# Kernel tuning notes

Measured on AMD Instinct MI355X. Metric: run time of the kernel, lower is better.

The kernel has to match this reference:

```python
import jax, jax.numpy as jnp
import numpy as np

N_NODES = 100000
N_EDGES = 800000
H_DIM = 128
E_DIM = 32
N_LAYER = 3


def setup_inputs() -> dict:
    key = jax.random.key(0)
    ks = jax.random.split(key, 5)
    x = jax.random.normal(ks[0], (N_NODES, H_DIM), dtype=jnp.float32)
    edge_index = jax.random.randint(ks[1], (2, N_EDGES), 0, N_NODES, dtype=jnp.int64)
    edge_attr = jax.random.normal(ks[2], (N_EDGES, E_DIM), dtype=jnp.float32)
    fan_in = 2 * H_DIM + E_DIM
    # torch Linear weight layout: [out_features, in_features]
    Wm = jax.random.normal(ks[3], (N_LAYER, H_DIM, fan_in), dtype=jnp.float32) / jnp.sqrt(fan_in)
    bm = jax.random.normal(ks[4], (N_LAYER, H_DIM), dtype=jnp.float32) * 0.01
    return {"x": x, "edge_index": edge_index, "edge_attr": edge_attr, "Wm": Wm, "bm": bm}


def reference(x, edge_index, edge_attr, Wm, bm):
    # PyG flow='source_to_target': row 0 = source (j), row 1 = target (i)
    src = edge_index[0]
    dst = edge_index[1]
    n_nodes = x.shape[0]
    n_layer = Wm.shape[0]
    for l in range(n_layer):  # small fixed layer count
        # message: m_ij = Linear(cat[x_j, x_i, edge_attr])
        m = jnp.concatenate([x[src], x[dst], edge_attr], axis=1)  # [E, 2h+e]
        m = jnp.einsum('ef,hf->eh', m, Wm[l]) + bm[l]             # [E, h]
        # aggr='add': scatter-add messages to target nodes
        x = jax.ops.segment_sum(m, dst, num_segments=n_nodes)     # [N, h]
        x = jax.nn.leaky_relu(x, negative_slope=0.01)
    # residual_connection='none' -> no-op; activate_last=True
    x = jax.nn.leaky_relu(x, negative_slope=0.01)
    return x
```

## Files before the change

kernel.cpp:

```cpp
#include <hip/hip_runtime.h>

#define N_NODES 100000
#define NP      100096
#define N_EDGES 800000
#define HD 128
#define ED 32
#define FAN 288
#define NL 3

#define SCHUNK 2048
#define SBLK   ((N_NODES + SCHUNK - 1) / SCHUNK)

typedef short bf16x8 __attribute__((ext_vector_type(8)));
typedef short bf16x4 __attribute__((ext_vector_type(4)));
typedef float f32x4  __attribute__((ext_vector_type(4)));

__device__ inline float b2f(short s) {
    unsigned u = ((unsigned)(unsigned short)s) << 16;
    return __builtin_bit_cast(float, u);
}
__device__ inline short f2b(float f) {
    unsigned u = __builtin_bit_cast(unsigned, f);
    unsigned r = u + 0x7FFFu + ((u >> 16) & 1u);
    return (short)(r >> 16);
}


__global__ void count_kernel(const int* __restrict__ dst, int* __restrict__ deg) {
    int e = blockIdx.x * 256 + threadIdx.x;
    if (e < N_EDGES) atomicAdd(&deg[dst[e]], 1);
}

__global__ void scan_reduce(const int* __restrict__ deg, int* __restrict__ bsum) {
    __shared__ int ws[4];
    const int tid = threadIdx.x;
    int i0 = blockIdx.x * SCHUNK + tid * 8;
    int t = 0;
    #pragma unroll
    for (int j = 0; j < 8; ++j) {
        int i = i0 + j;
        if (i < N_NODES) t += deg[i];
    }
    #pragma unroll
    for (int off = 32; off >= 1; off >>= 1) t += __shfl_down(t, off, 64);
    if ((tid & 63) == 0) ws[tid >> 6] = t;
    __syncthreads();
    if (tid == 0) bsum[blockIdx.x] = ws[0] + ws[1] + ws[2] + ws[3];
}

__global__ void scan_mid(const int* __restrict__ bsum, int* __restrict__ boff,
                         int* __restrict__ ptr) {
    int lane = threadIdx.x;
    int v = (lane < SBLK) ? bsum[lane] : 0;
    int s = v;
    #pragma unroll
    for (int off = 1; off < 64; off <<= 1) {
        int t = __shfl_up(s, off, 64);
        if (lane >= off) s += t;
    }
    if (lane < SBLK) boff[lane] = s - v;
    if (lane == 63) ptr[N_NODES] = s;
}

__global__ void scan_final(const int* __restrict__ deg, const int* __restrict__ boff,
                           int* __restrict__ ptr, int* __restrict__ cursor) {
    __shared__ int wsum[4];
    const int tid = threadIdx.x;
    const int lane = tid & 63, wid = tid >> 6;
    int i0 = blockIdx.x * SCHUNK + tid * 8;
    int v[8]; int tsum = 0;
    #pragma unroll
    for (int j = 0; j < 8; ++j) {
        int i = i0 + j;
        v[j] = (i < N_NODES) ? deg[i] : 0;
        tsum += v[j];
    }
    int s = tsum;
    #pragma unroll
    for (int off = 1; off < 64; off <<= 1) {
        int t = __shfl_up(s, off, 64);
        if (lane >= off) s += t;
    }
    if (lane == 63) wsum[wid] = s;
    __syncthreads();
    int woff = 0;
    #pragma unroll
    for (int w = 0; w < 4; ++w) if (w < wid) woff += wsum[w];
    int excl = boff[blockIdx.x] + woff + (s - tsum);
    #pragma unroll
    for (int j = 0; j < 8; ++j) {
        int i = i0 + j;
        if (i < N_NODES) { ptr[i] = excl; cursor[i] = excl; }
        excl += v[j];
    }
}

__global__ void fill_kernel(const int* __restrict__ src, const int* __restrict__ dst,
                            int* __restrict__ cursor, int2* __restrict__ csr2) {
    int e = blockIdx.x * 256 + threadIdx.x;
    if (e < N_EDGES) {
        int d = dst[e];
        int slot = atomicAdd(&cursor[d], 1);
        csr2[slot] = make_int2(src[e], e);
    }
}

__global__ void edge_sum(const int2* __restrict__ csr2, const int* __restrict__ ptr,
                         const float* __restrict__ eattr,
                         short* __restrict__ agge, float* __restrict__ degf) {
    int node = blockIdx.x * 32 + (threadIdx.x >> 3);
    int g = threadIdx.x & 7;
    if (node >= N_NODES) return;
    int s0 = ptr[node], s1 = ptr[node + 1];
    float4 a0 = make_float4(0.f,0.f,0.f,0.f), a1 = make_float4(0.f,0.f,0.f,0.f);
    int s = s0;
    int e0 = (s     < s1) ? csr2[s].y     : 0;
    int e1 = (s + 1 < s1) ? csr2[s + 1].y : 0;
    int e2 = (s + 2 < s1) ? csr2[s + 2].y : 0;
    int e3 = (s + 3 < s1) ? csr2[s + 3].y : 0;
    while (s + 4 <= s1) {
        float4 v0 = *reinterpret_cast<const float4*>(eattr + (size_t)e0 * ED + g * 4);
        float4 v1 = *reinterpret_cast<const float4*>(eattr + (size_t)e1 * ED + g * 4);
        float4 v2 = *reinterpret_cast<const float4*>(eattr + (size_t)e2 * ED + g * 4);
        float4 v3 = *reinterpret_cast<const float4*>(eattr + (size_t)e3 * ED + g * 4);
        s += 4;
        e0 = (s     < s1) ? csr2[s].y     : 0;
        e1 = (s + 1 < s1) ? csr2[s + 1].y : 0;
        e2 = (s + 2 < s1) ? csr2[s + 2].y : 0;
        e3 = (s + 3 < s1) ? csr2[s + 3].y : 0;
        a0.x += v0.x; a0.y += v0.y; a0.z += v0.z; a0.w += v0.w;
        a1.x += v1.x; a1.y += v1.y; a1.z += v1.z; a1.w += v1.w;
        a0.x += v2.x; a0.y += v2.y; a0.z += v2.z; a0.w += v2.w;
        a1.x += v3.x; a1.y += v3.y; a1.z += v3.z; a1.w += v3.w;
    }
    int rem = s1 - s;
    if (rem > 0) {
        float4 v = *reinterpret_cast<const float4*>(eattr + (size_t)e0 * ED + g * 4);
        a0.x += v.x; a0.y += v.y; a0.z += v.z; a0.w += v.w;
    }
    if (rem > 1) {
        float4 v = *reinterpret_cast<const float4*>(eattr + (size_t)e1 * ED + g * 4);
        a1.x += v.x; a1.y += v.y; a1.z += v.z; a1.w += v.w;
    }
    if (rem > 2) {
        float4 v = *reinterpret_cast<const float4*>(eattr + (size_t)e2 * ED + g * 4);
        a0.x += v.x; a0.y += v.y; a0.z += v.z; a0.w += v.w;
    }
    bf16x4 o;
    o[0] = f2b(a0.x + a1.x); o[1] = f2b(a0.y + a1.y);
    o[2] = f2b(a0.z + a1.z); o[3] = f2b(a0.w + a1.w);
    *reinterpret_cast<bf16x4*>(agge + (size_t)node * ED + g * 4) = o;
    if (g == 0) degf[node] = (float)(s1 - s0);
}

__global__ void wconv_kernel(const float* __restrict__ Wm, short* __restrict__ Wb) {
    int idx = blockIdx.x * 256 + threadIdx.x;
    if (idx < NL * HD * FAN) Wb[idx] = f2b(Wm[idx]);
}

__global__ void xconv_kernel(const float* __restrict__ x, const float* __restrict__ degf,
                             short* __restrict__ xb, short* __restrict__ xd) {
    int i4 = blockIdx.x * 256 + threadIdx.x;
    if (i4 >= N_NODES * (HD / 4)) return;
    int row = i4 >> 5;
    float d = degf[row];
    float4 v = reinterpret_cast<const float4*>(x)[i4];
    bf16x4 o, od;
    float vv[4] = {v.x, v.y, v.z, v.w};
    #pragma unroll
    for (int j = 0; j < 4; ++j) {
        short s = f2b(vv[j]);
        o[j] = s;
        od[j] = f2b(b2f(s) * d);
    }
    *reinterpret_cast<bf16x4*>(xb + (size_t)i4 * 4) = o;
    *reinterpret_cast<bf16x4*>(xd + (size_t)i4 * 4) = od;
}

#define TM 32

__global__ __launch_bounds__(256) void fused_layer(
    const int* __restrict__ ptr, const int2* __restrict__ csr2,
    const short* __restrict__ xprev,
    const short* __restrict__ xdeg,
    const short* __restrict__ agge,
    const float* __restrict__ degf,
    const short* __restrict__ Wb,
    const float* __restrict__ b,
    float* __restrict__ out_f32,
    short* __restrict__ out_x,
    short* __restrict__ out_xd,
    int last)
{
    __shared__ char As[TM * 256];
    const int tid = threadIdx.x;
    const int m0 = blockIdx.x * TM;

    {
        const int ng = tid >> 4, g = tid & 15;
        #pragma unroll
        for (int i = 0; i < 2; ++i) {
            int row = i * 16 + ng;
            int node = m0 + row;
            float acc0[8] = {}, acc1[8] = {};
            if (node < N_NODES) {
                int s0 = ptr[node], s1 = ptr[node + 1];
                int s = s0;
                int i0 = (s     < s1) ? csr2[s].x     : 0;
                int i1 = (s + 1 < s1) ? csr2[s + 1].x : 0;
                int i2 = (s + 2 < s1) ? csr2[s + 2].x : 0;
                int i3 = (s + 3 < s1) ? csr2[s + 3].x : 0;
                while (s + 4 <= s1) {
                    bf16x8 v0 = *reinterpret_cast<const bf16x8*>(xprev + (size_t)i0 * HD + g * 8);
                    bf16x8 v1 = *reinterpret_cast<const bf16x8*>(xprev + (size_t)i1 * HD + g * 8);
                    bf16x8 v2 = *reinterpret_cast<const bf16x8*>(xprev + (size_t)i2 * HD + g * 8);
                    bf16x8 v3 = *reinterpret_cast<const bf16x8*>(xprev + (size_t)i3 * HD + g * 8);
                    s += 4;
                    i0 = (s     < s1) ? csr2[s].x     : 0;
                    i1 = (s + 1 < s1) ? csr2[s + 1].x : 0;
                    i2 = (s + 2 < s1) ? csr2[s + 2].x : 0;
                    i3 = (s + 3 < s1) ? csr2[s + 3].x : 0;
                    #pragma unroll
                    for (int j = 0; j < 8; ++j) acc0[j] += b2f(v0[j]);
                    #pragma unroll
                    for (int j = 0; j < 8; ++j) acc1[j] += b2f(v1[j]);
                    #pragma unroll
                    for (int j = 0; j < 8; ++j) acc0[j] += b2f(v2[j]);
                    #pragma unroll
                    for (int j = 0; j < 8; ++j) acc1[j] += b2f(v3[j]);
                }
                int rem = s1 - s;
                if (rem > 0) {
                    bf16x8 v = *reinterpret_cast<const bf16x8*>(xprev + (size_t)i0 * HD + g * 8);
                    #pragma unroll
                    for (int j = 0; j < 8; ++j) acc0[j] += b2f(v[j]);
                }
                if (rem > 1) {
                    bf16x8 v = *reinterpret_cast<const bf16x8*>(xprev + (size_t)i1 * HD + g * 8);
                    #pragma unroll
                    for (int j = 0; j < 8; ++j) acc1[j] += b2f(v[j]);
                }
                if (rem > 2) {
                    bf16x8 v = *reinterpret_cast<const bf16x8*>(xprev + (size_t)i2 * HD + g * 8);
                    #pragma unroll
                    for (int j = 0; j < 8; ++j) acc0[j] += b2f(v[j]);
                }
            }
            bf16x8 o;
            #pragma unroll
            for (int j = 0; j < 8; ++j) o[j] = f2b(acc0[j] + acc1[j]);
            int byte = row * 256 + g * 16;
            byte ^= (row & 7) << 4;
            *reinterpret_cast<bf16x8*>(As + byte) = o;
        }
    }
    __syncthreads();

    const int w = tid >> 6, lane = tid & 63;
    const int l15 = lane & 15, lq = lane >> 4;
    const int kb = lq * 8;

    f32x4 acc[2][2];
    #pragma unroll
    for (int i = 0; i < 2; ++i)
        #pragma unroll
        for (int j = 0; j < 2; ++j) acc[i][j] = (f32x4){0.f, 0.f, 0.f, 0.f};

    #pragma unroll
    for (int kt = 0; kt < 4; ++kt) {
        bf16x8 a[2], bf[2];
        #pragma unroll
        for (int mf = 0; mf < 2; ++mf) {
            int row = mf * 16 + l15;
            int byte = row * 256 + kt * 64 + kb * 2;
            byte ^= (row & 7) << 4;
            a[mf] = *reinterpret_cast<const bf16x8*>(As + byte);
        }
        #pragma unroll
        for (int nf = 0; nf < 2; ++nf) {
            int c = w * 32 + nf * 16 + l15;
            bf[nf] = *reinterpret_cast<const bf16x8*>(Wb + (size_t)c * FAN + kt * 32 + kb);
        }
        #pragma unroll
        for (int mf = 0; mf < 2; ++mf)
            #pragma unroll
            for (int nf = 0; nf < 2; ++nf)
                acc[mf][nf] = __builtin_amdgcn_mfma_f32_16x16x32_bf16(
                    a[mf], bf[nf], acc[mf][nf], 0, 0, 0);
    }
    #pragma unroll
    for (int kt = 4; kt < 9; ++kt) {
        bf16x8 a[2], bf[2];
        #pragma unroll
        for (int mf = 0; mf < 2; ++mf) {
            size_t arow = (size_t)(m0 + mf * 16 + l15);
            a[mf] = (kt < 8)
                ? *reinterpret_cast<const bf16x8*>(xdeg + arow * HD + (kt * 32 - 128) + kb)
                : *reinterpret_cast<const bf16x8*>(agge + arow * ED + kb);
        }
        #pragma unroll
        for (int nf = 0; nf < 2; ++nf) {
            int c = w * 32 + nf * 16 + l15;
            bf[nf] = *reinterpret_cast<const bf16x8*>(Wb + (size_t)c * FAN + kt * 32 + kb);
        }
        #pragma unroll
        for (int mf = 0; mf < 2; ++mf)
            #pragma unroll
            for (int nf = 0; nf < 2; ++nf)
                acc[mf][nf] = __builtin_amdgcn_mfma_f32_16x16x32_bf16(
                    a[mf], bf[nf], acc[mf][nf], 0, 0, 0);
    }

    #pragma unroll
    for (int mf = 0; mf < 2; ++mf) {
        int r0 = m0 + mf * 16 + lq * 4;
        float dg[4];
        #pragma unroll
        for (int j = 0; j < 4; ++j)
            dg[j] = (r0 + j < N_NODES) ? degf[r0 + j] : 0.f;
        #pragma unroll
        for (int nf = 0; nf < 2; ++nf) {
            int c = w * 32 + nf * 16 + l15;
            float bc = b[c];
            #pragma unroll
            for (int j = 0; j < 4; ++j) {
                int row = r0 + j;
                if (row >= N_NODES) continue;
                float v = acc[mf][nf][j] + dg[j] * bc;
                v = (v >= 0.f) ? v : 0.01f * v;
                if (last) {
                    v = (v >= 0.f) ? v : 0.01f * v;
                    out_f32[(size_t)row * HD + c] = v;
                } else {
                    short xb = f2b(v);
                    out_x[(size_t)row * HD + c] = xb;
                    out_xd[(size_t)row * HD + c] = f2b(b2f(xb) * dg[j]);
                }
            }
        }
    }
}

extern "C" void kernel_launch(void* const* d_in, const int* in_sizes, int n_in,
                              void* d_out, int out_size, void* d_ws, size_t ws_size,
                              hipStream_t stream) {
    const float* x_in  = (const float*)d_in[0];
    const int*   ei    = (const int*)d_in[1];
    const float* eattr = (const float*)d_in[2];
    const float* Wm    = (const float*)d_in[3];
    const float* bm    = (const float*)d_in[4];
    float* out = (float*)d_out;

    char* ws = (char*)d_ws;
    size_t off = 0;
    auto alloc = [&](size_t bytes) -> void* {
        void* p = ws + off;
        off = (off + bytes + 255) & ~(size_t)255;
        return p;
    };
    short* x0     = (short*)alloc((size_t)NP * HD * 2);
    short* x1     = (short*)alloc((size_t)NP * HD * 2);
    short* xdeg   = (short*)alloc((size_t)NP * HD * 2);
    short* agge   = (short*)alloc((size_t)NP * ED * 2);
    float* degf   = (float*)alloc((size_t)NP * 4);
    int*   deg    = (int*)alloc((size_t)N_NODES * 4);
    int*   ptr    = (int*)alloc((size_t)(N_NODES + 1) * 4);
    int*   cursor = (int*)alloc((size_t)N_NODES * 4);
    int2*  csr2   = (int2*)alloc((size_t)N_EDGES * 8);
    short* Wb     = (short*)alloc((size_t)NL * HD * FAN * 2);
    int*   bsum   = (int*)alloc((size_t)SBLK * 4);
    int*   boff   = (int*)alloc((size_t)SBLK * 4);

    const int* src = ei;
    const int* dst = ei + N_EDGES;

    hipMemsetAsync(deg, 0, (size_t)N_NODES * 4, stream);
    count_kernel<<<(N_EDGES + 255) / 256, 256, 0, stream>>>(dst, deg);
    scan_reduce<<<SBLK, 256, 0, stream>>>(deg, bsum);
    scan_mid<<<1, 64, 0, stream>>>(bsum, boff, ptr);
    scan_final<<<SBLK, 256, 0, stream>>>(deg, boff, ptr, cursor);
    fill_kernel<<<(N_EDGES + 255) / 256, 256, 0, stream>>>(src, dst, cursor, csr2);
    edge_sum<<<(N_NODES + 31) / 32, 256, 0, stream>>>(csr2, ptr, eattr, agge, degf);
    wconv_kernel<<<(NL * HD * FAN + 255) / 256, 256, 0, stream>>>(Wm, Wb);
    xconv_kernel<<<(N_NODES * (HD / 4) + 255) / 256, 256, 0, stream>>>(x_in, degf, x0, xdeg);

    short* xping[2] = {x0, x1};
    for (int l = 0; l < NL; ++l) {
        fused_layer<<<NP / TM, 256, 0, stream>>>(
            ptr, csr2, xping[l & 1], xdeg, agge, degf,
            Wb + (size_t)l * HD * FAN, bm + (size_t)l * HD,
            out, xping[(l + 1) & 1], xdeg, (l == NL - 1) ? 1 : 0);
    }
}
```

Measured before the change: 344.1 us.

## Persistent atomic-ticket layer kernel, drop xdeg buffer, merge scan and conversion kernels

The node-layer kernel becomes persistent: a fixed grid takes 32-row tiles from an atomic ticket counter, with launch bounds set to 6 blocks per CU. The self term is now accumulated separately and scaled by degree in the epilogue, so the degree-scaled copy of x (xdeg) no longer has to be written each layer. The gather loop is unrolled from 4 to 6 neighbours, scan_mid is folded into scan_final, and the weight and x conversions are merged into one kernel. Together these cut kernel launches and memory traffic, at the cost of extra accumulator registers, ticket atomics, and a shift from bf16 rounding of x*deg to fp32 scaling.

```diff
diff --git a/kernel.cpp b/kernel.cpp
--- a/kernel.cpp
+++ b/kernel.cpp
@@ -11,6 +11,10 @@
 #define SCHUNK 2048
 #define SBLK   ((N_NODES + SCHUNK - 1) / SCHUNK)
 
+#define TM 32
+#define NTILES (NP / TM)
+#define PGRID  1536
+
 typedef short bf16x8 __attribute__((ext_vector_type(8)));
 typedef short bf16x4 __attribute__((ext_vector_type(4)));
 typedef float f32x4  __attribute__((ext_vector_type(4)));
@@ -48,25 +52,28 @@
     if (tid == 0) bsum[blockIdx.x] = ws[0] + ws[1] + ws[2] + ws[3];
 }
 
-__global__ void scan_mid(const int* __restrict__ bsum, int* __restrict__ boff,
-                         int* __restrict__ ptr) {
-    int lane = threadIdx.x;
-    int v = (lane < SBLK) ? bsum[lane] : 0;
-    int s = v;
-    #pragma unroll
-    for (int off = 1; off < 64; off <<= 1) {
-        int t = __shfl_up(s, off, 64);
-        if (lane >= off) s += t;
-    }
-    if (lane < SBLK) boff[lane] = s - v;
-    if (lane == 63) ptr[N_NODES] = s;
-}
-
-__global__ void scan_final(const int* __restrict__ deg, const int* __restrict__ boff,
+__global__ void scan_final(const int* __restrict__ deg, const int* __restrict__ bsum,
                            int* __restrict__ ptr, int* __restrict__ cursor) {
     __shared__ int wsum[4];
+    __shared__ int s_boff;
     const int tid = threadIdx.x;
     const int lane = tid & 63, wid = tid >> 6;
+    if (wid == 0) {
+        int v = (lane < SBLK) ? bsum[lane] : 0;
+        int s = v;
+        #pragma unroll
+        for (int off = 1; off < 64; off <<= 1) {
+            int t = __shfl_up(s, off, 64);
+            if (lane >= off) s += t;
+        }
+        int srcl = (blockIdx.x == 0) ? 0 : (int)blockIdx.x - 1;
+        int bprev = __shfl(s, srcl, 64);
+        if (lane == 0) s_boff = (blockIdx.x == 0) ? 0 : bprev;
+        int total = __shfl(s, SBLK - 1, 64);
+        if (blockIdx.x == 0 && lane == 0) ptr[N_NODES] = total;
+    }
+    __syncthreads();
+
     int i0 = blockIdx.x * SCHUNK + tid * 8;
     int v[8]; int tsum = 0;
     #pragma unroll
@@ -86,7 +93,7 @@
     int woff = 0;
     #pragma unroll
     for (int w = 0; w < 4; ++w) if (w < wid) woff += wsum[w];
-    int excl = boff[blockIdx.x] + woff + (s - tsum);
+    int excl = s_boff + woff + (s - tsum);
     #pragma unroll
     for (int j = 0; j < 8; ++j) {
         int i = i0 + j;
@@ -153,188 +160,186 @@
     if (g == 0) degf[node] = (float)(s1 - s0);
 }
 
-__global__ void wconv_kernel(const float* __restrict__ Wm, short* __restrict__ Wb) {
-    int idx = blockIdx.x * 256 + threadIdx.x;
-    if (idx < NL * HD * FAN) Wb[idx] = f2b(Wm[idx]);
-}
-
-__global__ void xconv_kernel(const float* __restrict__ x, const float* __restrict__ degf,
-                             short* __restrict__ xb, short* __restrict__ xd) {
+#define NW4 (NL * HD * FAN / 4)
+#define NX4 (N_NODES * (HD / 4))
+__global__ void conv_kernel(const float* __restrict__ Wm, short* __restrict__ Wb,
+                            const float* __restrict__ x, short* __restrict__ xb) {
     int i4 = blockIdx.x * 256 + threadIdx.x;
-    if (i4 >= N_NODES * (HD / 4)) return;
-    int row = i4 >> 5;
-    float d = degf[row];
-    float4 v = reinterpret_cast<const float4*>(x)[i4];
-    bf16x4 o, od;
-    float vv[4] = {v.x, v.y, v.z, v.w};
-    #pragma unroll
-    for (int j = 0; j < 4; ++j) {
-        short s = f2b(vv[j]);
-        o[j] = s;
-        od[j] = f2b(b2f(s) * d);
-    }
-    *reinterpret_cast<bf16x4*>(xb + (size_t)i4 * 4) = o;
-    *reinterpret_cast<bf16x4*>(xd + (size_t)i4 * 4) = od;
-}
-
-#define TM 32
-
-__global__ __launch_bounds__(256) void fused_layer(
+    if (i4 < NW4) {
+        float4 v = reinterpret_cast<const float4*>(Wm)[i4];
+        bf16x4 o;
+        o[0] = f2b(v.x); o[1] = f2b(v.y); o[2] = f2b(v.z); o[3] = f2b(v.w);
+        reinterpret_cast<bf16x4*>(Wb)[i4] = o;
+    }
+    int j4 = i4 - NW4;
+    if (j4 >= 0 && j4 < NX4) {
+        float4 v = reinterpret_cast<const float4*>(x)[j4];
+        bf16x4 o;
+        o[0] = f2b(v.x); o[1] = f2b(v.y); o[2] = f2b(v.z); o[3] = f2b(v.w);
+        reinterpret_cast<bf16x4*>(xb)[j4] = o;
+    }
+}
+
+__global__ __launch_bounds__(256, 6) void fused_layer(
     const int* __restrict__ ptr, const int2* __restrict__ csr2,
     const short* __restrict__ xprev,
-    const short* __restrict__ xdeg,
     const short* __restrict__ agge,
     const float* __restrict__ degf,
     const short* __restrict__ Wb,
     const float* __restrict__ b,
     float* __restrict__ out_f32,
     short* __restrict__ out_x,
-    short* __restrict__ out_xd,
+    int* __restrict__ tick,
     int last)
 {
     __shared__ char As[TM * 256];
+    __shared__ int s_tile;
     const int tid = threadIdx.x;
-    const int m0 = blockIdx.x * TM;
-
-    {
-        const int ng = tid >> 4, g = tid & 15;
-        #pragma unroll
-        for (int i = 0; i < 2; ++i) {
-            int row = i * 16 + ng;
-            int node = m0 + row;
-            float acc0[8] = {}, acc1[8] = {};
-            if (node < N_NODES) {
-                int s0 = ptr[node], s1 = ptr[node + 1];
-                int s = s0;
-                int i0 = (s     < s1) ? csr2[s].x     : 0;
-                int i1 = (s + 1 < s1) ? csr2[s + 1].x : 0;
-                int i2 = (s + 2 < s1) ? csr2[s + 2].x : 0;
-                int i3 = (s + 3 < s1) ? csr2[s + 3].x : 0;
-                while (s + 4 <= s1) {
-                    bf16x8 v0 = *reinterpret_cast<const bf16x8*>(xprev + (size_t)i0 * HD + g * 8);
-                    bf16x8 v1 = *reinterpret_cast<const bf16x8*>(xprev + (size_t)i1 * HD + g * 8);
-                    bf16x8 v2 = *reinterpret_cast<const bf16x8*>(xprev + (size_t)i2 * HD + g * 8);
-                    bf16x8 v3 = *reinterpret_cast<const bf16x8*>(xprev + (size_t)i3 * HD + g * 8);
-                    s += 4;
-                    i0 = (s     < s1) ? csr2[s].x     : 0;
-                    i1 = (s + 1 < s1) ? csr2[s + 1].x : 0;
-                    i2 = (s + 2 < s1) ? csr2[s + 2].x : 0;
-                    i3 = (s + 3 < s1) ? csr2[s + 3].x : 0;
+
+    for (;;) {
+        if (tid == 0) s_tile = atomicAdd(tick, 1);
+        __syncthreads();
+        const int tile = s_tile;
+        if (tile >= NTILES) return;
+        const int m0 = tile * TM;
+
+        {
+            const int ng = tid >> 4, g = tid & 15;
+            #pragma unroll
+            for (int i = 0; i < 2; ++i) {
+                int row = i * 16 + ng;
+                int node = m0 + row;
+                float acc0[8] = {}, acc1[8] = {};
+                if (node < N_NODES) {
+                    int s0 = ptr[node], s1 = ptr[node + 1];
+                    int s = s0;
+                    int id[6];
                     #pragma unroll
-                    for (int j = 0; j < 8; ++j) acc0[j] += b2f(v0[j]);
+                    for (int q = 0; q < 6; ++q) id[q] = (s + q < s1) ? csr2[s + q].x : 0;
+                    while (s + 6 <= s1) {
+                        bf16x8 v[6];
+                        #pragma unroll
+                        for (int q = 0; q < 6; ++q)
+                            v[q] = *reinterpret_cast<const bf16x8*>(
+                                xprev + (size_t)id[q] * HD + g * 8);
+                        s += 6;
+                        #pragma unroll
+                        for (int q = 0; q < 6; ++q) id[q] = (s + q < s1) ? csr2[s + q].x : 0;
+                        #pragma unroll
+                        for (int q = 0; q < 6; ++q) {
+                            float* ac = (q & 1) ? acc1 : acc0;
+                            #pragma unroll
+                            for (int j = 0; j < 8; ++j) ac[j] += b2f(v[q][j]);
+                        }
+                    }
+                    int rem = s1 - s;
                     #pragma unroll
-                    for (int j = 0; j < 8; ++j) acc1[j] += b2f(v1[j]);
-                    #pragma unroll
-                    for (int j = 0; j < 8; ++j) acc0[j] += b2f(v2[j]);
-                    #pragma unroll
-                    for (int j = 0; j < 8; ++j) acc1[j] += b2f(v3[j]);
+                    for (int q = 0; q < 5; ++q) {
+                        if (q < rem) {
+                            bf16x8 v = *reinterpret_cast<const bf16x8*>(
+                                xprev + (size_t)id[q] * HD + g * 8);
+                            float* ac = (q & 1) ? acc1 : acc0;
+                            #pragma unroll
+                            for (int j = 0; j < 8; ++j) ac[j] += b2f(v[j]);
+                        }
+                    }
                 }
-                int rem = s1 - s;
-                if (rem > 0) {
-                    bf16x8 v = *reinterpret_cast<const bf16x8*>(xprev + (size_t)i0 * HD + g * 8);
-                    #pragma unroll
-                    for (int j = 0; j < 8; ++j) acc0[j] += b2f(v[j]);
+                bf16x8 o;
+                #pragma unroll
+                for (int j = 0; j < 8; ++j) o[j] = f2b(acc0[j] + acc1[j]);
+                int byte = row * 256 + g * 16;
+                byte ^= (row & 7) << 4;
+                *reinterpret_cast<bf16x8*>(As + byte) = o;
+            }
+        }
+        __syncthreads();
+
+        const int w = tid >> 6, lane = tid & 63;
+        const int l15 = lane & 15, lq = lane >> 4;
+        const int kb = lq * 8;
+
+        f32x4 acc1[2][2], acc2[2][2];
+        #pragma unroll
+        for (int i = 0; i < 2; ++i)
+            #pragma unroll
+            for (int j = 0; j < 2; ++j) {
+                acc1[i][j] = (f32x4){0.f, 0.f, 0.f, 0.f};
+                acc2[i][j] = (f32x4){0.f, 0.f, 0.f, 0.f};
+            }
+
+        #pragma unroll
+        for (int kt = 0; kt < 4; ++kt) {
+            bf16x8 a[2], bf[2];
+            #pragma unroll
+            for (int mf = 0; mf < 2; ++mf) {
+                int row = mf * 16 + l15;
+                int byte = row * 256 + kt * 64 + kb * 2;
+                byte ^= (row & 7) << 4;
+                a[mf] = *reinterpret_cast<const bf16x8*>(As + byte);
+            }
+            #pragma unroll
+            for (int nf = 0; nf < 2; ++nf) {
+                int c = w * 32 + nf * 16 + l15;
+                bf[nf] = *reinterpret_cast<const bf16x8*>(Wb + (size_t)c * FAN + kt * 32 + kb);
+            }
+            #pragma unroll
+            for (int mf = 0; mf < 2; ++mf)
+                #pragma unroll
+                for (int nf = 0; nf < 2; ++nf)
+                    acc1[mf][nf] = __builtin_amdgcn_mfma_f32_16x16x32_bf16(
+                        a[mf], bf[nf], acc1[mf][nf], 0, 0, 0);
+        }
+        #pragma unroll
+        for (int kt = 4; kt < 9; ++kt) {
+            bf16x8 a[2], bf[2];
+            #pragma unroll
+            for (int mf = 0; mf < 2; ++mf) {
+                size_t arow = (size_t)(m0 + mf * 16 + l15);
+                a[mf] = (kt < 8)
+                    ? *reinterpret_cast<const bf16x8*>(xprev + arow * HD + (kt * 32 - 128) + kb)
+                    : *reinterpret_cast<const bf16x8*>(agge + arow * ED + kb);
+            }
+            #pragma unroll
+            for (int nf = 0; nf < 2; ++nf) {
+                int c = w * 32 + nf * 16 + l15;
+                bf[nf] = *reinterpret_cast<const bf16x8*>(Wb + (size_t)c * FAN + kt * 32 + kb);
+            }
+            #pragma unroll
+            for (int mf = 0; mf < 2; ++mf)
+                #pragma unroll
+                for (int nf = 0; nf < 2; ++nf) {
+                    if (kt < 8)
+                        acc2[mf][nf] = __builtin_amdgcn_mfma_f32_16x16x32_bf16(
+                            a[mf], bf[nf], acc2[mf][nf], 0, 0, 0);
+                    else
+                        acc1[mf][nf] = __builtin_amdgcn_mfma_f32_16x16x32_bf16(
+                            a[mf], bf[nf], acc1[mf][nf], 0, 0, 0);
                 }
-                if (rem > 1) {
-                    bf16x8 v = *reinterpret_cast<const bf16x8*>(xprev + (size_t)i1 * HD + g * 8);
-                    #pragma unroll
-                    for (int j = 0; j < 8; ++j) acc1[j] += b2f(v[j]);
-                }
-                if (rem > 2) {
-                    bf16x8 v = *reinterpret_cast<const bf16x8*>(xprev + (size_t)i2 * HD + g * 8);
-                    #pragma unroll
-                    for (int j = 0; j < 8; ++j) acc0[j] += b2f(v[j]);
-                }
-            }
-            bf16x8 o;
-            #pragma unroll
-            for (int j = 0; j < 8; ++j) o[j] = f2b(acc0[j] + acc1[j]);
-            int byte = row * 256 + g * 16;
-            byte ^= (row & 7) << 4;
-            *reinterpret_cast<bf16x8*>(As + byte) = o;
-        }
-    }
-    __syncthreads();
-
-    const int w = tid >> 6, lane = tid & 63;
-    const int l15 = lane & 15, lq = lane >> 4;
-    const int kb = lq * 8;
-
-    f32x4 acc[2][2];
-    #pragma unroll
-    for (int i = 0; i < 2; ++i)
-        #pragma unroll
-        for (int j = 0; j < 2; ++j) acc[i][j] = (f32x4){0.f, 0.f, 0.f, 0.f};
-
-    #pragma unroll
-    for (int kt = 0; kt < 4; ++kt) {
-        bf16x8 a[2], bf[2];
+        }
+
         #pragma unroll
         for (int mf = 0; mf < 2; ++mf) {
-            int row = mf * 16 + l15;
-            int byte = row * 256 + kt * 64 + kb * 2;
-            byte ^= (row & 7) << 4;
-            a[mf] = *reinterpret_cast<const bf16x8*>(As + byte);
-        }
-        #pragma unroll
-        for (int nf = 0; nf < 2; ++nf) {
-            int c = w * 32 + nf * 16 + l15;
-            bf[nf] = *reinterpret_cast<const bf16x8*>(Wb + (size_t)c * FAN + kt * 32 + kb);
-        }
-        #pragma unroll
-        for (int mf = 0; mf < 2; ++mf)
-            #pragma unroll
-            for (int nf = 0; nf < 2; ++nf)
-                acc[mf][nf] = __builtin_amdgcn_mfma_f32_16x16x32_bf16(
-                    a[mf], bf[nf], acc[mf][nf], 0, 0, 0);
-    }
-    #pragma unroll
-    for (int kt = 4; kt < 9; ++kt) {
-        bf16x8 a[2], bf[2];
-        #pragma unroll
-        for (int mf = 0; mf < 2; ++mf) {
-            size_t arow = (size_t)(m0 + mf * 16 + l15);
-            a[mf] = (kt < 8)
-                ? *reinterpret_cast<const bf16x8*>(xdeg + arow * HD + (kt * 32 - 128) + kb)
-                : *reinterpret_cast<const bf16x8*>(agge + arow * ED + kb);
-        }
-        #pragma unroll
-        for (int nf = 0; nf < 2; ++nf) {
-            int c = w * 32 + nf * 16 + l15;
-            bf[nf] = *reinterpret_cast<const bf16x8*>(Wb + (size_t)c * FAN + kt * 32 + kb);
-        }
-        #pragma unroll
-        for (int mf = 0; mf < 2; ++mf)
-            #pragma unroll
-            for (int nf = 0; nf < 2; ++nf)
-                acc[mf][nf] = __builtin_amdgcn_mfma_f32_16x16x32_bf16(
-                    a[mf], bf[nf], acc[mf][nf], 0, 0, 0);
-    }
-
-    #pragma unroll
-    for (int mf = 0; mf < 2; ++mf) {
-        int r0 = m0 + mf * 16 + lq * 4;
-        float dg[4];
-        #pragma unroll
-        for (int j = 0; j < 4; ++j)
-            dg[j] = (r0 + j < N_NODES) ? degf[r0 + j] : 0.f;
-        #pragma unroll
-        for (int nf = 0; nf < 2; ++nf) {
-            int c = w * 32 + nf * 16 + l15;
-            float bc = b[c];
-            #pragma unroll
-            for (int j = 0; j < 4; ++j) {
-                int row = r0 + j;
-                if (row >= N_NODES) continue;
-                float v = acc[mf][nf][j] + dg[j] * bc;
-                v = (v >= 0.f) ? v : 0.01f * v;
-                if (last) {
+            int r0 = m0 + mf * 16 + lq * 4;
+            float dg[4];
+            #pragma unroll
+            for (int j = 0; j < 4; ++j)
+                dg[j] = (r0 + j < N_NODES) ? degf[r0 + j] : 0.f;
+            #pragma unroll
+            for (int nf = 0; nf < 2; ++nf) {
+                int c = w * 32 + nf * 16 + l15;
+                float bc = b[c];
+                #pragma unroll
+                for (int j = 0; j < 4; ++j) {
+                    int row = r0 + j;
+                    if (row >= N_NODES) continue;
+                    float v = acc1[mf][nf][j] + dg[j] * (acc2[mf][nf][j] + bc);
                     v = (v >= 0.f) ? v : 0.01f * v;
-                    out_f32[(size_t)row * HD + c] = v;
-                } else {
-                    short xb = f2b(v);
-                    out_x[(size_t)row * HD + c] = xb;
-                    out_xd[(size_t)row * HD + c] = f2b(b2f(xb) * dg[j]);
+                    if (last) {
+                        v = (v >= 0.f) ? v : 0.01f * v;
+                        out_f32[(size_t)row * HD + c] = v;
+                    } else {
+                        out_x[(size_t)row * HD + c] = f2b(v);
+                    }
                 }
             }
         }
@@ -358,37 +363,34 @@
         off = (off + bytes + 255) & ~(size_t)255;
         return p;
     };
-    short* x0     = (short*)alloc((size_t)NP * HD * 2);
-    short* x1     = (short*)alloc((size_t)NP * HD * 2);
-    short* xdeg   = (short*)alloc((size_t)NP * HD * 2);
-    short* agge   = (short*)alloc((size_t)NP * ED * 2);
-    float* degf   = (float*)alloc((size_t)NP * 4);
-    int*   deg    = (int*)alloc((size_t)N_NODES * 4);
-    int*   ptr    = (int*)alloc((size_t)(N_NODES + 1) * 4);
-    int*   cursor = (int*)alloc((size_t)N_NODES * 4);
-    int2*  csr2   = (int2*)alloc((size_t)N_EDGES * 8);
-    short* Wb     = (short*)alloc((size_t)NL * HD * FAN * 2);
-    int*   bsum   = (int*)alloc((size_t)SBLK * 4);
-    int*   boff   = (int*)alloc((size_t)SBLK * 4);
+    short* x0      = (short*)alloc((size_t)NP * HD * 2);
+    short* x1      = (short*)alloc((size_t)NP * HD * 2);
+    short* agge    = (short*)alloc((size_t)NP * ED * 2);
+    float* degf    = (float*)alloc((size_t)NP * 4);
+    int*   deg     = (int*)alloc((size_t)N_NODES * 4);
+    int*   tickets = (int*)alloc(256);
+    int*   ptr     = (int*)alloc((size_t)(N_NODES + 1) * 4);
+    int*   cursor  = (int*)alloc((size_t)N_NODES * 4);
+    int2*  csr2    = (int2*)alloc((size_t)N_EDGES * 8);
+    short* Wb      = (short*)alloc((size_t)NL * HD * FAN * 2);
+    int*   bsum    = (int*)alloc((size_t)SBLK * 4);
 
     const int* src = ei;
     const int* dst = ei + N_EDGES;
 
-    hipMemsetAsync(deg, 0, (size_t)N_NODES * 4, stream);
+    hipMemsetAsync(deg, 0, (size_t)((char*)tickets - (char*)deg) + 64, stream);
     count_kernel<<<(N_EDGES + 255) / 256, 256, 0, stream>>>(dst, deg);
     scan_reduce<<<SBLK, 256, 0, stream>>>(deg, bsum);
-    scan_mid<<<1, 64, 0, stream>>>(bsum, boff, ptr);
-    scan_final<<<SBLK, 256, 0, stream>>>(deg, boff, ptr, cursor);
+    scan_final<<<SBLK, 256, 0, stream>>>(deg, bsum, ptr, cursor);
     fill_kernel<<<(N_EDGES + 255) / 256, 256, 0, stream>>>(src, dst, cursor, csr2);
     edge_sum<<<(N_NODES + 31) / 32, 256, 0, stream>>>(csr2, ptr, eattr, agge, degf);
-    wconv_kernel<<<(NL * HD * FAN + 255) / 256, 256, 0, stream>>>(Wm, Wb);
-    xconv_kernel<<<(N_NODES * (HD / 4) + 255) / 256, 256, 0, stream>>>(x_in, degf, x0, xdeg);
+    conv_kernel<<<(NW4 + NX4 + 255) / 256, 256, 0, stream>>>(Wm, Wb, x_in, x0);
 
     short* xping[2] = {x0, x1};
     for (int l = 0; l < NL; ++l) {
-        fused_layer<<<NP / TM, 256, 0, stream>>>(
-            ptr, csr2, xping[l & 1], xdeg, agge, degf,
+        fused_layer<<<PGRID, 256, 0, stream>>>(
+            ptr, csr2, xping[l & 1], agge, degf,
             Wb + (size_t)l * HD * FAN, bm + (size_t)l * HD,
-            out, xping[(l + 1) & 1], xdeg, (l == NL - 1) ? 1 : 0);
-    }
-}
+            out, xping[(l + 1) & 1], tickets + l, (l == NL - 1) ? 1 : 0);
+    }
+}
```

Result: slower. 424.6 us (+23.4%).
